# Optimization experiments

Hardware: AMD Instinct MI355X
Metric: run time of the kernel (lower is better)

## Reference

```python
import jax, jax.numpy as jnp
import numpy as np
from jax import lax

D, H, DK, L, FF, V, B, S = 384, 12, 32, 6, 1536, 30522, 16, 512

def _logit(p):
    return float(np.log(p / (1.0 - p)))

def setup_inputs():
    key = jax.random.key(0)
    ks = jax.random.split(key, 16)
    def g(i, shape, scale=0.02):
        return jax.random.normal(ks[i], shape, jnp.float32) * scale
    return {
        "input_ids": jax.random.randint(ks[0], (B, S), 0, V),
        "attention_mask": jnp.ones((B, S), jnp.int32),
        "emb_tok": g(1, (V, D)),
        "emb_pos": g(2, (S, D)),
        "emb_type": g(3, (2, D)),
        "emb_ln_g": jnp.ones((D,), jnp.float32),
        "emb_ln_b": jnp.zeros((D,), jnp.float32),
        "Wq": g(4, (L, D, D)), "bq": jnp.zeros((L, D), jnp.float32),
        "Wk": g(5, (L, D, D)), "bk": jnp.zeros((L, D), jnp.float32),
        "Wv": g(6, (L, D, D)), "bv": jnp.zeros((L, D), jnp.float32),
        "Wbeta": g(7, (L, D, H)), "bbeta": jnp.zeros((L, H), jnp.float32),
        "decay_fast": jnp.full((L, H), _logit(0.3), jnp.float32),
        "decay_slow": jnp.full((L, H), _logit(0.85), jnp.float32),
        "mix_logit": jnp.zeros((L, H), jnp.float32),
        "Wg": g(8, (L, D, D)),
        "Wo": g(9, (L, D, D)), "bo": jnp.zeros((L, D), jnp.float32),
        "attn_ln_g": jnp.ones((L, D), jnp.float32), "attn_ln_b": jnp.zeros((L, D), jnp.float32),
        "Wffn1": g(10, (L, D, FF)), "bffn1": jnp.zeros((L, FF), jnp.float32),
        "Wffn2": g(11, (L, FF, D)), "bffn2": jnp.zeros((L, D), jnp.float32),
        "ffn_ln_g": jnp.ones((L, D), jnp.float32), "ffn_ln_b": jnp.zeros((L, D), jnp.float32),
    }

def _ln(x, g, b, eps=1e-12):
    m = x.mean(-1, keepdims=True)
    v = ((x - m) ** 2).mean(-1, keepdims=True)
    return (x - m) * lax.rsqrt(v + eps) * g + b

def _delta_attn(x, mask_f, Wq, bq, Wk, bk, Wv, bv, Wbeta, bbeta, df_logit, ds_logit, mix_logit, Wg, Wo, bo):
    # Hierarchical delta-rule linear attention: O(n) recurrence, two decay timescales.
    Bz, Sq, _ = x.shape
    q = jax.nn.silu((x @ Wq + bq).reshape(Bz, Sq, H, DK))
    k = jax.nn.silu((x @ Wk + bk).reshape(Bz, Sq, H, DK))
    k = k / (jnp.linalg.norm(k, axis=-1, keepdims=True) + 1e-6)
    v = (x @ Wv + bv).reshape(Bz, Sq, H, DK)
    beta = jax.nn.sigmoid(x @ Wbeta + bbeta) * mask_f[..., None]  # [B,S,H]
    df = jax.nn.sigmoid(df_logit)[None, :, None, None]  # fast decay, per head
    ds = jax.nn.sigmoid(ds_logit)[None, :, None, None]  # slow decay, per head
    qT = q.transpose(1, 0, 2, 3)  # time-major [S,B,H,DK]
    kT = k.transpose(1, 0, 2, 3)
    vT = v.transpose(1, 0, 2, 3)
    betaT = beta.transpose(1, 0, 2)

    def step(carry, xs):
        Sf, Ss = carry  # [B,H,DK,DK] fast/slow memory states
        kt, vt, qt, bt = xs
        err_f = (vt - jnp.einsum('bhk,bhkv->bhv', kt, Sf)) * bt[..., None]
        Sf = df * Sf + jnp.einsum('bhk,bhv->bhkv', kt, err_f)
        err_s = (vt - jnp.einsum('bhk,bhkv->bhv', kt, Ss)) * bt[..., None]
        Ss = ds * Ss + jnp.einsum('bhk,bhv->bhkv', kt, err_s)
        of = jnp.einsum('bhk,bhkv->bhv', qt, Sf)
        os = jnp.einsum('bhk,bhkv->bhv', qt, Ss)
        return (Sf, Ss), (of, os)

    S0 = jnp.zeros((Bz, H, DK, DK), x.dtype)
    _, (ofT, osT) = lax.scan(step, (S0, S0), (kT, vT, qT, betaT))
    mix = jax.nn.sigmoid(mix_logit)[None, None, :, None]
    o = mix * ofT.transpose(1, 0, 2, 3) + (1.0 - mix) * osT.transpose(1, 0, 2, 3)
    o = o.reshape(Bz, Sq, D)
    o = o * jax.nn.sigmoid(x @ Wg)  # enhanced-flux output gate
    return o @ Wo + bo

def reference(input_ids, attention_mask, emb_tok, emb_pos, emb_type, emb_ln_g, emb_ln_b, Wq, bq, Wk, bk, Wv, bv, Wbeta, bbeta, decay_fast, decay_slow, mix_logit, Wg, Wo, bo, attn_ln_g, attn_ln_b, Wffn1, bffn1, Wffn2, bffn2, ffn_ln_g, ffn_ln_b):
    mask_f = attention_mask.astype(jnp.float32)
    h = emb_tok[input_ids] + emb_pos[None, :input_ids.shape[1]] + emb_type[0][None, None]
    h = _ln(h, emb_ln_g, emb_ln_b)
    for i in range(L):
        attn = _delta_attn(h, mask_f, Wq[i], bq[i], Wk[i], bk[i], Wv[i], bv[i], Wbeta[i], bbeta[i], decay_fast[i], decay_slow[i], mix_logit[i], Wg[i], Wo[i], bo[i])
        h = _ln(h + attn, attn_ln_g[i], attn_ln_b[i])
        ffn = jax.nn.gelu(h @ Wffn1[i] + bffn1[i], approximate=False) @ Wffn2[i] + bffn2[i]
        h = _ln(h + ffn, ffn_ln_g[i], ffn_ln_b[i])
    m = mask_f[..., None]
    emb = (h * m).sum(1) / jnp.clip(m.sum(1), 1e-9)
    return emb / (jnp.linalg.norm(emb, axis=1, keepdims=True) + 1e-12)
```

## Files before the change

kernel.cpp:

```cpp
#include <hip/hip_runtime.h>
#include <hip/hip_bf16.h>

#define NTOK   8192
#define DMODEL 384
#define NHEAD  12
#define DHEAD  32
#define NLAYER 6
#define DFF    1536
#define SEQ    512
#define BATCH  16
#define WTAL   1916928L

typedef __attribute__((ext_vector_type(8))) short short8;
typedef __attribute__((ext_vector_type(4))) float f32x4;

__device__ __forceinline__ float sigmoidf_(float x){ return 1.f/(1.f+expf(-x)); }

__device__ __forceinline__ ushort f2b(float x){
  uint b = __builtin_bit_cast(uint, x);
  uint r = (b + 0x7FFFu + ((b>>16)&1u)) >> 16;
  return (ushort)r;
}
__device__ __forceinline__ uint pk2(float lo, float hi){
  return (uint)f2b(lo) | ((uint)f2b(hi)<<16);
}
__device__ __forceinline__ float4 b2f4(uint2 u){
  float4 f;
  f.x = __builtin_bit_cast(float, u.x<<16);
  f.y = __builtin_bit_cast(float, u.x & 0xffff0000u);
  f.z = __builtin_bit_cast(float, u.y<<16);
  f.w = __builtin_bit_cast(float, u.y & 0xffff0000u);
  return f;
}
__device__ __forceinline__ float red8(float x){
  int t = __builtin_amdgcn_update_dpp(0, __builtin_bit_cast(int,x), 0xB1, 0xF, 0xF, true);
  x += __builtin_bit_cast(float,t);
  t = __builtin_amdgcn_update_dpp(0, __builtin_bit_cast(int,x), 0x4E, 0xF, 0xF, true);
  x += __builtin_bit_cast(float,t);
  t = __builtin_amdgcn_update_dpp(0, __builtin_bit_cast(int,x), 0x141, 0xF, 0xF, true);
  x += __builtin_bit_cast(float,t);
  return x;
}
__device__ __forceinline__ void gload16(const ushort* g, ushort* l){
  __builtin_amdgcn_global_load_lds((const __attribute__((address_space(1))) void*)g,
                                   (__attribute__((address_space(3))) void*)l, 16, 0, 0);
}

__global__ __launch_bounds__(128) void embed_ln_kernel(
    const int* __restrict__ ids, const float* __restrict__ tok,
    const float* __restrict__ pos, const float* __restrict__ typ,
    const float* __restrict__ g, const float* __restrict__ bvec,
    float* __restrict__ out, ushort* __restrict__ outb)
{
  int n = blockIdx.x;
  int t = n & (SEQ-1);
  int id = ids[n];
  int tid = threadIdx.x;
  float v[3]; float s1=0.f, s2=0.f;
  #pragma unroll
  for (int j=0;j<3;j++){
    int d = tid + j*128;
    float x = tok[(long)id*DMODEL + d] + pos[t*DMODEL + d] + typ[d];
    v[j]=x; s1+=x; s2+=x*x;
  }
  #pragma unroll
  for (int m=1;m<64;m<<=1){ s1 += __shfl_xor(s1,m); s2 += __shfl_xor(s2,m); }
  __shared__ float r1[2], r2[2];
  if ((tid&63)==0){ r1[tid>>6]=s1; r2[tid>>6]=s2; }
  __syncthreads();
  s1 = r1[0]+r1[1]; s2 = r2[0]+r2[1];
  float mean = s1*(1.f/DMODEL);
  float var  = s2*(1.f/DMODEL) - mean*mean;
  float inv  = rsqrtf(var + 1e-12f);
  #pragma unroll
  for (int j=0;j<3;j++){
    int d = tid + j*128;
    float y = (v[j]-mean)*inv*g[d] + bvec[d];
    out[(long)n*DMODEL + d] = y;
    outb[(long)n*DMODEL + d] = f2b(y);
  }
}

__global__ __launch_bounds__(128) void add_ln_kernel(
    float* __restrict__ h, const float* __restrict__ res,
    const float* __restrict__ g, const float* __restrict__ bvec,
    ushort* __restrict__ hb)
{
  int n = blockIdx.x;
  int tid = threadIdx.x;
  float v[3]; float s1=0.f, s2=0.f;
  #pragma unroll
  for (int j=0;j<3;j++){
    int d = tid + j*128;
    float x = h[(long)n*DMODEL + d] + res[(long)n*DMODEL + d];
    v[j]=x; s1+=x; s2+=x*x;
  }
  #pragma unroll
  for (int m=1;m<64;m<<=1){ s1 += __shfl_xor(s1,m); s2 += __shfl_xor(s2,m); }
  __shared__ float r1[2], r2[2];
  if ((tid&63)==0){ r1[tid>>6]=s1; r2[tid>>6]=s2; }
  __syncthreads();
  s1 = r1[0]+r1[1]; s2 = r2[0]+r2[1];
  float mean = s1*(1.f/DMODEL);
  float var  = s2*(1.f/DMODEL) - mean*mean;
  float inv  = rsqrtf(var + 1e-12f);
  #pragma unroll
  for (int j=0;j<3;j++){
    int d = tid + j*128;
    float y = (v[j]-mean)*inv*g[d] + bvec[d];
    h[(long)n*DMODEL + d] = y;
    hb[(long)n*DMODEL + d] = f2b(y);
  }
}

__global__ __launch_bounds__(256) void tcvt6(
    const float* __restrict__ Wq, const float* __restrict__ Wk,
    const float* __restrict__ Wv, const float* __restrict__ Wg,
    const float* __restrict__ Wo, const float* __restrict__ W1,
    const float* __restrict__ W2, ushort* __restrict__ WTA)
{
  __shared__ float tile[32][33];
  int l = blockIdx.x / 1872;
  int bid = blockIdx.x % 1872;
  const float* Wq_l = Wq + (long)l*DMODEL*DMODEL;
  const float* Wk_l = Wk + (long)l*DMODEL*DMODEL;
  const float* Wv_l = Wv + (long)l*DMODEL*DMODEL;
  const float* Wg_l = Wg + (long)l*DMODEL*DMODEL;
  const float* Wo_l = Wo + (long)l*DMODEL*DMODEL;
  const float* W1_l = W1 + (long)l*DMODEL*DFF;
  const float* W2_l = W2 + (long)l*DFF*DMODEL;
  ushort* WTAl = WTA + (long)l*WTAL;

  const float* src; long dstbase; int rowlen, Nd, tk, tn, row0;
  if (bid < 720){
    int seg = bid/144, t = bid%144;
    tk = t%12; tn = t/12;
    src = (seg==0)?Wq_l:(seg==1)?Wk_l:(seg==2)?Wv_l:(seg==3)?Wg_l:Wo_l;
    Nd = 384; rowlen = 384;
    if (seg<4){ dstbase=0; row0=seg*384; }
    else      { dstbase=589824; row0=0; }
  } else if (bid < 1296){
    int t = bid-720; tk=t%12; tn=t/12;
    src=W1_l; Nd=DFF; dstbase=737280; row0=0; rowlen=384;
  } else {
    int t = bid-1296; tk=t%48; tn=t/48;
    src=W2_l; Nd=384; dstbase=1327104; row0=0; rowlen=DFF;
  }
  int k0=tk*32, n0=tn*32;
  int tt=threadIdx.x;
  int r=tt>>3, c4=(tt&7)<<2;
  const float* sp = src + (long)(k0+r)*Nd + n0 + c4;
  float4 f = *(const float4*)sp;
  tile[r][c4+0]=f.x; tile[r][c4+1]=f.y; tile[r][c4+2]=f.z; tile[r][c4+3]=f.w;
  __syncthreads();
  ushort4 o;
  o.x=f2b(tile[c4+0][r]); o.y=f2b(tile[c4+1][r]);
  o.z=f2b(tile[c4+2][r]); o.w=f2b(tile[c4+3][r]);
  *(ushort4*)(WTAl + dstbase + (long)(row0+n0+r)*rowlen + k0 + c4) = o;
}

__device__ __forceinline__ int2 xcd_swz(){
  int lin = blockIdx.y*64 + blockIdx.x;
  int nb = gridDim.x*gridDim.y;
  int s = (lin & 7)*(nb>>3) + (lin>>3);
  return make_int2(s & 63, s >> 6);
}

template<int ACT, int OUTBF>
__global__ __launch_bounds__(256) void gemm_bf(
    const ushort* __restrict__ Xb, const ushort* __restrict__ WT,
    const float* __restrict__ bias, void* __restrict__ Cv, int Kd, int Nd)
{
  __shared__ ushort A_lds[128*32];
  __shared__ ushort B_lds[128*32];
  int tid = threadIdx.x;
  int2 bxy = xcd_swz();
  int bm = bxy.x*128, bn = bxy.y*128;
  int w = tid>>6, lane = tid&63;
  int wm = w>>1, wn = w&1;
  f32x4 acc[4][4];
  #pragma unroll
  for (int i=0;i<4;i++)
    #pragma unroll
    for (int j=0;j<4;j++) acc[i][j]=(f32x4)(0.f);

  int cl = lane&15, koff = (lane>>4)*8;
  int srow = w*32 + (lane>>2);
  int scol = (lane&3)*8;
  const ushort* gA0 = Xb + (long)(bm+srow)*Kd + scol;
  const ushort* gA1 = gA0 + 16*(long)Kd;
  const ushort* gB0 = WT + (long)(bn+srow)*Kd + scol;
  const ushort* gB1 = gB0 + 16*(long)Kd;
  ushort* lA = A_lds + w*1024;
  ushort* lB = B_lds + w*1024;

  for (int k0=0; k0<Kd; k0+=32){
    gload16(gA0+k0, lA);
    gload16(gA1+k0, lA+512);
    gload16(gB0+k0, lB);
    gload16(gB1+k0, lB+512);
    __syncthreads();
    short8 bf[4];
    #pragma unroll
    for (int ni=0;ni<4;ni++)
      bf[ni] = *(const short8*)&B_lds[(wn*64+ni*16+cl)*32 + koff];
    #pragma unroll
    for (int mi=0;mi<4;mi++){
      short8 af = *(const short8*)&A_lds[(wm*64+mi*16+cl)*32 + koff];
      #pragma unroll
      for (int ni=0;ni<4;ni++)
        acc[mi][ni] = __builtin_amdgcn_mfma_f32_16x16x32_bf16(af, bf[ni], acc[mi][ni], 0,0,0);
    }
    __syncthreads();
  }

  int rb = (lane>>4)*4;
  #pragma unroll
  for (int ni=0; ni<4; ni++){
    int col = bn + wn*64 + ni*16 + cl;
    float bsv = bias ? bias[col] : 0.f;
    #pragma unroll
    for (int mi=0; mi<4; mi++){
      #pragma unroll
      for (int j=0;j<4;j++){
        int row = bm + wm*64 + mi*16 + rb + j;
        float c = acc[mi][ni][j] + bsv;
        if (ACT==1)      c = c*sigmoidf_(c);
        else if (ACT==2) c = 0.5f*c*(1.f+erff(c*0.70710678118f));
        else if (ACT==3) c = sigmoidf_(c);
        if (OUTBF) ((ushort*)Cv)[(long)row*Nd + col] = f2b(c);
        else       ((float*)Cv)[(long)row*Nd + col] = c;
      }
    }
  }
}

template<int ACT, int OUTBF>
__global__ __launch_bounds__(256) void gemm_bf2(
    const ushort* __restrict__ Xb, const ushort* __restrict__ WT,
    const float* __restrict__ bias, void* __restrict__ Cv, int Kd, int Nd)
{
  __shared__ ushort A_lds[128*32];
  __shared__ ushort B_lds[64*32];
  int tid = threadIdx.x;
  int2 bxy = xcd_swz();
  int bm = bxy.x*128, bn = bxy.y*64;
  int w = tid>>6, lane = tid&63;
  int wm = w>>1, wn = w&1;
  f32x4 acc[4][2];
  #pragma unroll
  for (int i=0;i<4;i++){ acc[i][0]=(f32x4)(0.f); acc[i][1]=(f32x4)(0.f); }

  int cl = lane&15, koff = (lane>>4)*8;
  int srowA = w*32 + (lane>>2);
  int scol = (lane&3)*8;
  const ushort* gA0 = Xb + (long)(bm+srowA)*Kd + scol;
  const ushort* gA1 = gA0 + 16*(long)Kd;
  int srowB = w*16 + (lane>>2);
  const ushort* gB = WT + (long)(bn+srowB)*Kd + scol;
  ushort* lA = A_lds + w*1024;
  ushort* lB = B_lds + w*512;

  for (int k0=0; k0<Kd; k0+=32){
    gload16(gA0+k0, lA);
    gload16(gA1+k0, lA+512);
    gload16(gB+k0, lB);
    __syncthreads();
    short8 b0 = *(const short8*)&B_lds[(wn*32+cl)*32 + koff];
    short8 b1 = *(const short8*)&B_lds[(wn*32+16+cl)*32 + koff];
    #pragma unroll
    for (int mi=0;mi<4;mi++){
      short8 af = *(const short8*)&A_lds[(wm*64+mi*16+cl)*32 + koff];
      acc[mi][0] = __builtin_amdgcn_mfma_f32_16x16x32_bf16(af, b0, acc[mi][0], 0,0,0);
      acc[mi][1] = __builtin_amdgcn_mfma_f32_16x16x32_bf16(af, b1, acc[mi][1], 0,0,0);
    }
    __syncthreads();
  }

  int rb = (lane>>4)*4;
  #pragma unroll
  for (int ni=0; ni<2; ni++){
    int col = bn + wn*32 + ni*16 + cl;
    float bsv = bias ? bias[col] : 0.f;
    #pragma unroll
    for (int mi=0; mi<4; mi++){
      #pragma unroll
      for (int j=0;j<4;j++){
        int row = bm + wm*64 + mi*16 + rb + j;
        float c = acc[mi][ni][j] + bsv;
        if (ACT==1)      c = c*sigmoidf_(c);
        else if (ACT==2) c = 0.5f*c*(1.f+erff(c*0.70710678118f));
        else if (ACT==3) c = sigmoidf_(c);
        if (OUTBF) ((ushort*)Cv)[(long)row*Nd + col] = f2b(c);
        else       ((float*)Cv)[(long)row*Nd + col] = c;
      }
    }
  }
}

__global__ __launch_bounds__(256) void gemm_qkvg(
    const ushort* __restrict__ Xb, const ushort* __restrict__ WT,
    const float* __restrict__ bq, const float* __restrict__ bk,
    const float* __restrict__ bv, ushort* __restrict__ C)
{
  __shared__ ushort A_lds[128*32];
  __shared__ ushort B_lds[128*32];
  int tid = threadIdx.x;
  int2 bxy = xcd_swz();
  int bm = bxy.x*128, bn = bxy.y*128;
  int w = tid>>6, lane = tid&63;
  int wm = w>>1, wn = w&1;
  f32x4 acc[4][4];
  #pragma unroll
  for (int i=0;i<4;i++)
    #pragma unroll
    for (int j=0;j<4;j++) acc[i][j]=(f32x4)(0.f);

  int cl = lane&15, koff = (lane>>4)*8;
  int srow = w*32 + (lane>>2);
  int scol = (lane&3)*8;
  const ushort* gA0 = Xb + (long)(bm+srow)*DMODEL + scol;
  const ushort* gA1 = gA0 + 16*DMODEL;
  const ushort* gB0 = WT + (long)(bn+srow)*DMODEL + scol;
  const ushort* gB1 = gB0 + 16*DMODEL;
  ushort* lA = A_lds + w*1024;
  ushort* lB = B_lds + w*1024;

  for (int k0=0; k0<DMODEL; k0+=32){
    gload16(gA0+k0, lA);
    gload16(gA1+k0, lA+512);
    gload16(gB0+k0, lB);
    gload16(gB1+k0, lB+512);
    __syncthreads();
    short8 bf[4];
    #pragma unroll
    for (int ni=0;ni<4;ni++)
      bf[ni] = *(const short8*)&B_lds[(wn*64+ni*16+cl)*32 + koff];
    #pragma unroll
    for (int mi=0;mi<4;mi++){
      short8 af = *(const short8*)&A_lds[(wm*64+mi*16+cl)*32 + koff];
      #pragma unroll
      for (int ni=0;ni<4;ni++)
        acc[mi][ni] = __builtin_amdgcn_mfma_f32_16x16x32_bf16(af, bf[ni], acc[mi][ni], 0,0,0);
    }
    __syncthreads();
  }

  int seg = bxy.y/3;
  const float* bp = (seg==0)?bq:(seg==1)?bk:(seg==2)?bv:nullptr;
  int boff = seg*384;
  int rb = (lane>>4)*4;
  #pragma unroll
  for (int ni=0; ni<4; ni++){
    int col = bn + wn*64 + ni*16 + cl;
    float bsv = bp ? bp[col-boff] : 0.f;
    #pragma unroll
    for (int mi=0; mi<4; mi++){
      #pragma unroll
      for (int j=0;j<4;j++){
        int row = bm + wm*64 + mi*16 + rb + j;
        float c = acc[mi][ni][j] + bsv;
        if (seg<2)       c = c*sigmoidf_(c);
        else if (seg==3) c = sigmoidf_(c);
        C[(long)row*DFF + col] = f2b(c);
      }
    }
  }
}

__global__ __launch_bounds__(384) void beta_kernel(
    const float* __restrict__ X, const float* __restrict__ Wb, const float* __restrict__ bb,
    const int* __restrict__ mask, float* __restrict__ Bb)
{
  __shared__ float xs[DMODEL];
  int n = blockIdx.x; int tid = threadIdx.x;
  xs[tid] = X[(long)n*DMODEL + tid];
  __syncthreads();
  int hh = tid >> 5, i = tid & 31;
  float s = 0.f;
  for (int d=i; d<DMODEL; d+=32) s += xs[d]*Wb[d*NHEAD+hh];
  #pragma unroll
  for (int m=1;m<32;m<<=1) s += __shfl_xor(s,m);
  if (i==0) Bb[n*NHEAD+hh] = (float)mask[n] * sigmoidf_(s + bb[hh]);
}

__global__ __launch_bounds__(512,2) void scan12_kernel(
    const ushort* __restrict__ QKVGb, const float* __restrict__ Bb,
    const float* __restrict__ dfl, const float* __restrict__ dsl,
    const float* __restrict__ mixl, ushort* __restrict__ OA)
{
  __shared__ float Qc[66][36], Kc[66][36], Vt[32][68], Bc[68], Ofs[2][64][36];
  int bh = blockIdx.x;
  int b = bh / NHEAD, hh = bh - b*NHEAD;
  int tid = threadIdx.x;
  int w = tid>>6, lane = tid&63;
  int st = w>>2, vq = w&3;
  int kq = lane&7, v = vq*8 + (lane>>3);
  float dec = sigmoidf_(st ? dsl[hh] : dfl[hh]);
  float mix = sigmoidf_(mixl[hh]);
  long rowbase = (long)b*SEQ;
  const ushort* rp = QKVGb + rowbase*DFF + hh*32;
  const float* bp = Bb + rowbase*NHEAD + hh;

  int r0 = tid>>3, c40 = (tid&7)<<2;
  float S[4] = {0.f,0.f,0.f,0.f};

  float4 sq, sk, sv; float sb = 0.f;
  {
    long g = (long)r0*DFF;
    sq = b2f4(*(const uint2*)(rp + g + c40));
    sk = b2f4(*(const uint2*)(rp + g + 384 + c40));
    sv = b2f4(*(const uint2*)(rp + g + 768 + c40));
    if (tid < 64) sb = bp[(long)tid*NHEAD];
    float ss = red8(sk.x*sk.x + sk.y*sk.y + sk.z*sk.z + sk.w*sk.w);
    float inv = 1.f/(sqrtf(ss)+1e-6f);
    sk.x*=inv; sk.y*=inv; sk.z*=inv; sk.w*=inv;
    *(float4*)&Qc[r0][c40] = sq;
    *(float4*)&Kc[r0][c40] = sk;
    Vt[c40+0][r0]=sv.x; Vt[c40+1][r0]=sv.y; Vt[c40+2][r0]=sv.z; Vt[c40+3][r0]=sv.w;
    if (tid < 64) Bc[tid] = sb;
  }
  __syncthreads();

  for (int c=0; c<8; ++c){
    if (c < 7){
      long g = (long)((c+1)*64 + r0)*DFF;
      sq = b2f4(*(const uint2*)(rp + g + c40));
      sk = b2f4(*(const uint2*)(rp + g + 384 + c40));
      sv = b2f4(*(const uint2*)(rp + g + 768 + c40));
      if (tid < 64) sb = bp[(long)((c+1)*64 + tid)*NHEAD];
    }
    float4 g4 = b2f4(*(const uint2*)(rp + (long)(c*64 + r0)*DFF + 1152 + c40));
    __builtin_amdgcn_sched_barrier(0);

    float4 kA = *(const float4*)&Kc[0][kq*4];
    float4 qA = *(const float4*)&Qc[0][kq*4];
    float4 kB = *(const float4*)&Kc[1][kq*4];
    float4 qB = *(const float4*)&Qc[1][kq*4];
    float vrA[4], brA[4], vrB[4], brB[4];
    *(float4*)vrA = *(const float4*)&Vt[v][0];
    *(float4*)brA = *(const float4*)&Bc[0];

    for (int t8=0; t8<8; ++t8){
      *(float4*)vrB = *(const float4*)&Vt[v][(2*t8+1)*4];
      *(float4*)brB = *(const float4*)&Bc[(2*t8+1)*4];
      #pragma unroll
      for (int i=0;i<4;i++){
        int t = t8*8 + i;
        float4 kN = *(const float4*)&Kc[t+2][kq*4];
        float4 qN = *(const float4*)&Qc[t+2][kq*4];
        float pa = kA.x*S[0] + kA.y*S[1];
        float pb = kA.z*S[2] + kA.w*S[3];
        float p = red8(pa+pb);
        float err = (vrA[i] - p)*brA[i];
        S[0] = dec*S[0] + kA.x*err;
        S[1] = dec*S[1] + kA.y*err;
        S[2] = dec*S[2] + kA.z*err;
        S[3] = dec*S[3] + kA.w*err;
        float oa = qA.x*S[0] + qA.y*S[1];
        float ob = qA.z*S[2] + qA.w*S[3];
        float o = red8(oa+ob);
        if (kq==0) Ofs[st][t][v] = o;
        kA=kB; qA=qB; kB=kN; qB=qN;
      }
      *(float4*)vrA = *(const float4*)&Vt[v][(2*t8+2)*4];
      *(float4*)brA = *(const float4*)&Bc[(2*t8+2)*4];
      #pragma unroll
      for (int i=0;i<4;i++){
        int t = t8*8 + 4 + i;
        float4 kN = *(const float4*)&Kc[t+2][kq*4];
        float4 qN = *(const float4*)&Qc[t+2][kq*4];
        float pa = kA.x*S[0] + kA.y*S[1];
        float pb = kA.z*S[2] + kA.w*S[3];
        float p = red8(pa+pb);
        float err = (vrB[i] - p)*brB[i];
        S[0] = dec*S[0] + kA.x*err;
        S[1] = dec*S[1] + kA.y*err;
        S[2] = dec*S[2] + kA.z*err;
        S[3] = dec*S[3] + kA.w*err;
        float oa = qA.x*S[0] + qA.y*S[1];
        float ob = qA.z*S[2] + qA.w*S[3];
        float o = red8(oa+ob);
        if (kq==0) Ofs[st][t][v] = o;
        kA=kB; qA=qB; kB=kN; qB=qN;
      }
    }
    __syncthreads();

    {
      float4 of = *(const float4*)&Ofs[0][r0][c40];
      float4 os = *(const float4*)&Ofs[1][r0][c40];
      float a0 = (mix*of.x + (1.f-mix)*os.x)*g4.x;
      float a1 = (mix*of.y + (1.f-mix)*os.y)*g4.y;
      float a2 = (mix*of.z + (1.f-mix)*os.z)*g4.z;
      float a3 = (mix*of.w + (1.f-mix)*os.w)*g4.w;
      uint2 o2; o2.x = pk2(a0,a1); o2.y = pk2(a2,a3);
      *(uint2*)(OA + (rowbase + c*64 + r0)*DMODEL + hh*32 + c40) = o2;
    }
    if (c < 7){
      *(float4*)&Qc[r0][c40] = sq;
      *(float4*)&Kc[r0][c40] = sk;
      Vt[c40+0][r0]=sv.x; Vt[c40+1][r0]=sv.y; Vt[c40+2][r0]=sv.z; Vt[c40+3][r0]=sv.w;
      if (tid < 64) Bc[tid] = sb;
    }
    __syncthreads();
  }
}

__global__ __launch_bounds__(384) void pool_norm_kernel(
    const float* __restrict__ h, const int* __restrict__ mask, float* __restrict__ out)
{
  int b = blockIdx.x; int d = threadIdx.x;
  float s=0.f, ms=0.f;
  for (int t=0;t<SEQ;t++){
    float m = (float)mask[b*SEQ+t];
    s += h[((long)b*SEQ+t)*DMODEL + d]*m;
    ms += m;
  }
  float emb = s / fmaxf(ms, 1e-9f);
  float ss = emb*emb;
  #pragma unroll
  for (int m2=1;m2<64;m2<<=1) ss += __shfl_xor(ss,m2);
  __shared__ float r[6];
  if ((d&63)==0) r[d>>6]=ss;
  __syncthreads();
  ss = r[0]+r[1]+r[2]+r[3]+r[4]+r[5];
  out[b*DMODEL+d] = emb / (sqrtf(ss)+1e-12f);
}

extern "C" void kernel_launch(void* const* d_in, const int* in_sizes, int n_in,
                              void* d_out, int out_size, void* d_ws, size_t ws_size,
                              hipStream_t stream)
{
  const int*   ids   = (const int*)d_in[0];
  const int*   amask = (const int*)d_in[1];
  const float* etok  = (const float*)d_in[2];
  const float* epos  = (const float*)d_in[3];
  const float* etyp  = (const float*)d_in[4];
  const float* elng  = (const float*)d_in[5];
  const float* elnb  = (const float*)d_in[6];
  const float* Wq = (const float*)d_in[7];  const float* bq = (const float*)d_in[8];
  const float* Wk = (const float*)d_in[9];  const float* bk = (const float*)d_in[10];
  const float* Wv = (const float*)d_in[11]; const float* bv = (const float*)d_in[12];
  const float* Wb = (const float*)d_in[13]; const float* bb = (const float*)d_in[14];
  const float* dfl = (const float*)d_in[15];
  const float* dsl = (const float*)d_in[16];
  const float* mixl= (const float*)d_in[17];
  const float* Wg = (const float*)d_in[18];
  const float* Wo = (const float*)d_in[19]; const float* bo = (const float*)d_in[20];
  const float* alng = (const float*)d_in[21]; const float* alnb = (const float*)d_in[22];
  const float* W1 = (const float*)d_in[23]; const float* b1 = (const float*)d_in[24];
  const float* W2 = (const float*)d_in[25]; const float* b2 = (const float*)d_in[26];
  const float* flng = (const float*)d_in[27]; const float* flnb = (const float*)d_in[28];

  float* ws = (float*)d_ws;
  const long TD = (long)NTOK*DMODEL;
  float* h      = ws;
  ushort* hbf   = (ushort*)(h + TD);
  ushort* QKVGb = (ushort*)(h + TD + TD/2);
  ushort* OA    = (ushort*)(h + TD + TD/2 + 2*TD);
  float* Rb     = h + TD + TD/2 + 2*TD + TD/2;
  float* Bb     = Rb + TD;
  ushort* WTA   = (ushort*)(Bb + (long)NTOK*NHEAD);
  ushort* F1B   = QKVGb;

  embed_ln_kernel<<<NTOK,128,0,stream>>>(ids, etok, epos, etyp, elng, elnb, h, hbf);
  tcvt6<<<6*1872,256,0,stream>>>(Wq, Wk, Wv, Wg, Wo, W1, W2, WTA);

  for (int l=0;l<NLAYER;l++){
    ushort* WTAl = WTA + (long)l*WTAL;
    gemm_qkvg<<<dim3(64,12),256,0,stream>>>(hbf, WTAl, bq+l*DMODEL, bk+l*DMODEL, bv+l*DMODEL, QKVGb);
    beta_kernel<<<NTOK,384,0,stream>>>(h, Wb + (long)l*DMODEL*NHEAD, bb + l*NHEAD, amask, Bb);
    scan12_kernel<<<BATCH*NHEAD,512,0,stream>>>(QKVGb, Bb, dfl + l*NHEAD, dsl + l*NHEAD, mixl + l*NHEAD, OA);
    gemm_bf2<0,0><<<dim3(64,6),256,0,stream>>>(OA, WTAl+589824, bo + l*DMODEL, Rb, DMODEL, DMODEL);
    add_ln_kernel<<<NTOK,128,0,stream>>>(h, Rb, alng + (long)l*DMODEL, alnb + (long)l*DMODEL, hbf);
    gemm_bf<2,1><<<dim3(64,12),256,0,stream>>>(hbf, WTAl+737280, b1 + (long)l*DFF, F1B, DMODEL, DFF);
    gemm_bf2<0,0><<<dim3(64,6),256,0,stream>>>(F1B, WTAl+1327104, b2 + (long)l*DMODEL, Rb, DFF, DMODEL);
    add_ln_kernel<<<NTOK,128,0,stream>>>(h, Rb, flng + (long)l*DMODEL, flnb + (long)l*DMODEL, hbf);
  }

  pool_norm_kernel<<<BATCH,384,0,stream>>>(h, amask, (float*)d_out);
}
```

Measured before the change: 1.365 ms.

## Fuse beta projection into LayerNorm kernels and widen scan to 1024 threads

Removes the standalone beta kernel by computing the next layer's beta gate inside the embedding LayerNorm and the FFN add-LayerNorm, reusing the normalized row already in registers. The delta-rule scan kernel is doubled to 1024 threads so each lane holds 2 state elements instead of 4, with 16-lane DPP reductions, and the Q/V and K/beta chunk loads are split across the two halves. This is meant to cut a launch and a re-read of h per layer and to shorten the serial per-step dependency chain in the scan. In exchange, LayerNorm kernels take extra shared memory and a reduction step, and the scan uses more threads and a longer reduction per step.

```diff
diff --git a/kernel.cpp b/kernel.cpp
--- a/kernel.cpp
+++ b/kernel.cpp
@@ -41,17 +41,62 @@
   x += __builtin_bit_cast(float,t);
   return x;
 }
+__device__ __forceinline__ float red16(float x){
+  int t = __builtin_amdgcn_update_dpp(0, __builtin_bit_cast(int,x), 0xB1, 0xF, 0xF, true);
+  x += __builtin_bit_cast(float,t);
+  t = __builtin_amdgcn_update_dpp(0, __builtin_bit_cast(int,x), 0x4E, 0xF, 0xF, true);
+  x += __builtin_bit_cast(float,t);
+  t = __builtin_amdgcn_update_dpp(0, __builtin_bit_cast(int,x), 0x141, 0xF, 0xF, true);
+  x += __builtin_bit_cast(float,t);
+  t = __builtin_amdgcn_update_dpp(0, __builtin_bit_cast(int,x), 0x140, 0xF, 0xF, true);
+  x += __builtin_bit_cast(float,t);
+  return x;
+}
 __device__ __forceinline__ void gload16(const ushort* g, ushort* l){
   __builtin_amdgcn_global_load_lds((const __attribute__((address_space(1))) void*)g,
                                    (__attribute__((address_space(3))) void*)l, 16, 0, 0);
+}
+
+__device__ __forceinline__ void beta_from_row(
+    int n, int tid, const float y0, const float y1, const float y2,
+    const float* __restrict__ Wb, const float* __restrict__ bbv,
+    const int* __restrict__ amask, float* __restrict__ Bb,
+    float (*bred)[13])
+{
+  float part[12];
+  #pragma unroll
+  for (int hh=0;hh<12;hh++) part[hh]=0.f;
+  #pragma unroll
+  for (int j=0;j<3;j++){
+    int d = tid + j*128;
+    float yv = (j==0)?y0:(j==1)?y1:y2;
+    const float* wrow = Wb + (long)d*12;
+    #pragma unroll
+    for (int hh=0;hh<12;hh++) part[hh] += yv * wrow[hh];
+  }
+  #pragma unroll
+  for (int hh=0;hh<12;hh++) bred[tid][hh] = part[hh];
+  __syncthreads();
+  if (tid < 96){
+    int hh = tid>>3, i = tid&7;
+    float s = 0.f;
+    #pragma unroll
+    for (int k=0;k<16;k++) s += bred[i + 8*k][hh];
+    s += __shfl_xor(s,1); s += __shfl_xor(s,2); s += __shfl_xor(s,4);
+    if (i==0) Bb[(long)n*NHEAD+hh] = (float)amask[n] * sigmoidf_(s + bbv[hh]);
+  }
 }
 
 __global__ __launch_bounds__(128) void embed_ln_kernel(
     const int* __restrict__ ids, const float* __restrict__ tok,
     const float* __restrict__ pos, const float* __restrict__ typ,
     const float* __restrict__ g, const float* __restrict__ bvec,
-    float* __restrict__ out, ushort* __restrict__ outb)
-{
+    float* __restrict__ out, ushort* __restrict__ outb,
+    const float* __restrict__ Wb0, const float* __restrict__ bb0,
+    const int* __restrict__ amask, float* __restrict__ Bb)
+{
+  __shared__ float r1[2], r2[2];
+  __shared__ float bred[128][13];
   int n = blockIdx.x;
   int t = n & (SEQ-1);
   int id = ids[n];
@@ -65,27 +110,33 @@
   }
   #pragma unroll
   for (int m=1;m<64;m<<=1){ s1 += __shfl_xor(s1,m); s2 += __shfl_xor(s2,m); }
-  __shared__ float r1[2], r2[2];
   if ((tid&63)==0){ r1[tid>>6]=s1; r2[tid>>6]=s2; }
   __syncthreads();
   s1 = r1[0]+r1[1]; s2 = r2[0]+r2[1];
   float mean = s1*(1.f/DMODEL);
   float var  = s2*(1.f/DMODEL) - mean*mean;
   float inv  = rsqrtf(var + 1e-12f);
+  float y[3];
   #pragma unroll
   for (int j=0;j<3;j++){
     int d = tid + j*128;
-    float y = (v[j]-mean)*inv*g[d] + bvec[d];
-    out[(long)n*DMODEL + d] = y;
-    outb[(long)n*DMODEL + d] = f2b(y);
-  }
+    y[j] = (v[j]-mean)*inv*g[d] + bvec[d];
+    out[(long)n*DMODEL + d] = y[j];
+    outb[(long)n*DMODEL + d] = f2b(y[j]);
+  }
+  __syncthreads();
+  beta_from_row(n, tid, y[0], y[1], y[2], Wb0, bb0, amask, Bb, bred);
 }
 
 __global__ __launch_bounds__(128) void add_ln_kernel(
     float* __restrict__ h, const float* __restrict__ res,
     const float* __restrict__ g, const float* __restrict__ bvec,
-    ushort* __restrict__ hb)
-{
+    ushort* __restrict__ hb,
+    const float* __restrict__ Wbn, const float* __restrict__ bbn,
+    const int* __restrict__ amask, float* __restrict__ Bb)
+{
+  __shared__ float r1[2], r2[2];
+  __shared__ float bred[128][13];
   int n = blockIdx.x;
   int tid = threadIdx.x;
   float v[3]; float s1=0.f, s2=0.f;
@@ -97,19 +148,23 @@
   }
   #pragma unroll
   for (int m=1;m<64;m<<=1){ s1 += __shfl_xor(s1,m); s2 += __shfl_xor(s2,m); }
-  __shared__ float r1[2], r2[2];
   if ((tid&63)==0){ r1[tid>>6]=s1; r2[tid>>6]=s2; }
   __syncthreads();
   s1 = r1[0]+r1[1]; s2 = r2[0]+r2[1];
   float mean = s1*(1.f/DMODEL);
   float var  = s2*(1.f/DMODEL) - mean*mean;
   float inv  = rsqrtf(var + 1e-12f);
+  float y[3];
   #pragma unroll
   for (int j=0;j<3;j++){
     int d = tid + j*128;
-    float y = (v[j]-mean)*inv*g[d] + bvec[d];
-    h[(long)n*DMODEL + d] = y;
-    hb[(long)n*DMODEL + d] = f2b(y);
+    y[j] = (v[j]-mean)*inv*g[d] + bvec[d];
+    h[(long)n*DMODEL + d] = y[j];
+    hb[(long)n*DMODEL + d] = f2b(y[j]);
+  }
+  if (Wbn){
+    __syncthreads();
+    beta_from_row(n, tid, y[0], y[1], y[2], Wbn, bbn, amask, Bb, bred);
   }
 }
 
@@ -368,23 +423,7 @@
   }
 }
 
-__global__ __launch_bounds__(384) void beta_kernel(
-    const float* __restrict__ X, const float* __restrict__ Wb, const float* __restrict__ bb,
-    const int* __restrict__ mask, float* __restrict__ Bb)
-{
-  __shared__ float xs[DMODEL];
-  int n = blockIdx.x; int tid = threadIdx.x;
-  xs[tid] = X[(long)n*DMODEL + tid];
-  __syncthreads();
-  int hh = tid >> 5, i = tid & 31;
-  float s = 0.f;
-  for (int d=i; d<DMODEL; d+=32) s += xs[d]*Wb[d*NHEAD+hh];
-  #pragma unroll
-  for (int m=1;m<32;m<<=1) s += __shfl_xor(s,m);
-  if (i==0) Bb[n*NHEAD+hh] = (float)mask[n] * sigmoidf_(s + bb[hh]);
-}
-
-__global__ __launch_bounds__(512,2) void scan12_kernel(
+__global__ __launch_bounds__(1024,4) void scan14_kernel(
     const ushort* __restrict__ QKVGb, const float* __restrict__ Bb,
     const float* __restrict__ dfl, const float* __restrict__ dsl,
     const float* __restrict__ mixl, ushort* __restrict__ OA)
@@ -394,49 +433,58 @@
   int b = bh / NHEAD, hh = bh - b*NHEAD;
   int tid = threadIdx.x;
   int w = tid>>6, lane = tid&63;
-  int st = w>>2, vq = w&3;
-  int kq = lane&7, v = vq*8 + (lane>>3);
+  int st = w>>3, vg = w&7;
+  int kq = lane&15, v = vg*4 + (lane>>4);
   float dec = sigmoidf_(st ? dsl[hh] : dfl[hh]);
-  float mix = sigmoidf_(mixl[hh]);
+  float mixv = sigmoidf_(mixl[hh]);
   long rowbase = (long)b*SEQ;
   const ushort* rp = QKVGb + rowbase*DFF + hh*32;
   const float* bp = Bb + rowbase*NHEAD + hh;
 
-  int r0 = tid>>3, c40 = (tid&7)<<2;
-  float S[4] = {0.f,0.f,0.f,0.f};
+  bool sideA = tid < 512;
+  int ts = sideA ? tid : (tid-512);
+  int r0 = ts>>3, c40 = (ts&7)<<2;
+  float S0=0.f, S1=0.f;
 
   float4 sq, sk, sv; float sb = 0.f;
   {
     long g = (long)r0*DFF;
-    sq = b2f4(*(const uint2*)(rp + g + c40));
-    sk = b2f4(*(const uint2*)(rp + g + 384 + c40));
-    sv = b2f4(*(const uint2*)(rp + g + 768 + c40));
-    if (tid < 64) sb = bp[(long)tid*NHEAD];
-    float ss = red8(sk.x*sk.x + sk.y*sk.y + sk.z*sk.z + sk.w*sk.w);
-    float inv = 1.f/(sqrtf(ss)+1e-6f);
-    sk.x*=inv; sk.y*=inv; sk.z*=inv; sk.w*=inv;
-    *(float4*)&Qc[r0][c40] = sq;
-    *(float4*)&Kc[r0][c40] = sk;
-    Vt[c40+0][r0]=sv.x; Vt[c40+1][r0]=sv.y; Vt[c40+2][r0]=sv.z; Vt[c40+3][r0]=sv.w;
-    if (tid < 64) Bc[tid] = sb;
+    if (sideA){
+      sq = b2f4(*(const uint2*)(rp + g + c40));
+      sv = b2f4(*(const uint2*)(rp + g + 768 + c40));
+      *(float4*)&Qc[r0][c40] = sq;
+      Vt[c40+0][r0]=sv.x; Vt[c40+1][r0]=sv.y; Vt[c40+2][r0]=sv.z; Vt[c40+3][r0]=sv.w;
+    } else {
+      sk = b2f4(*(const uint2*)(rp + g + 384 + c40));
+      if (ts < 64) sb = bp[(long)ts*NHEAD];
+      float ss = red8(sk.x*sk.x + sk.y*sk.y + sk.z*sk.z + sk.w*sk.w);
+      float inv = 1.f/(sqrtf(ss)+1e-6f);
+      sk.x*=inv; sk.y*=inv; sk.z*=inv; sk.w*=inv;
+      *(float4*)&Kc[r0][c40] = sk;
+      if (ts < 64) Bc[ts] = sb;
+    }
   }
   __syncthreads();
 
   for (int c=0; c<8; ++c){
+    float4 g4;
     if (c < 7){
       long g = (long)((c+1)*64 + r0)*DFF;
-      sq = b2f4(*(const uint2*)(rp + g + c40));
-      sk = b2f4(*(const uint2*)(rp + g + 384 + c40));
-      sv = b2f4(*(const uint2*)(rp + g + 768 + c40));
-      if (tid < 64) sb = bp[(long)((c+1)*64 + tid)*NHEAD];
-    }
-    float4 g4 = b2f4(*(const uint2*)(rp + (long)(c*64 + r0)*DFF + 1152 + c40));
+      if (sideA){
+        sq = b2f4(*(const uint2*)(rp + g + c40));
+        sv = b2f4(*(const uint2*)(rp + g + 768 + c40));
+      } else {
+        sk = b2f4(*(const uint2*)(rp + g + 384 + c40));
+        if (ts < 64) sb = bp[(long)((c+1)*64 + ts)*NHEAD];
+      }
+    }
+    if (!sideA) g4 = b2f4(*(const uint2*)(rp + (long)(c*64 + r0)*DFF + 1152 + c40));
     __builtin_amdgcn_sched_barrier(0);
 
-    float4 kA = *(const float4*)&Kc[0][kq*4];
-    float4 qA = *(const float4*)&Qc[0][kq*4];
-    float4 kB = *(const float4*)&Kc[1][kq*4];
-    float4 qB = *(const float4*)&Qc[1][kq*4];
+    float2 kA = *(const float2*)&Kc[0][kq*2];
+    float2 qA = *(const float2*)&Qc[0][kq*2];
+    float2 kB = *(const float2*)&Kc[1][kq*2];
+    float2 qB = *(const float2*)&Qc[1][kq*2];
     float vrA[4], brA[4], vrB[4], brB[4];
     *(float4*)vrA = *(const float4*)&Vt[v][0];
     *(float4*)brA = *(const float4*)&Bc[0];
@@ -447,19 +495,13 @@
       #pragma unroll
       for (int i=0;i<4;i++){
         int t = t8*8 + i;
-        float4 kN = *(const float4*)&Kc[t+2][kq*4];
-        float4 qN = *(const float4*)&Qc[t+2][kq*4];
-        float pa = kA.x*S[0] + kA.y*S[1];
-        float pb = kA.z*S[2] + kA.w*S[3];
-        float p = red8(pa+pb);
+        float2 kN = *(const float2*)&Kc[t+2][kq*2];
+        float2 qN = *(const float2*)&Qc[t+2][kq*2];
+        float p = red16(kA.x*S0 + kA.y*S1);
         float err = (vrA[i] - p)*brA[i];
-        S[0] = dec*S[0] + kA.x*err;
-        S[1] = dec*S[1] + kA.y*err;
-        S[2] = dec*S[2] + kA.z*err;
-        S[3] = dec*S[3] + kA.w*err;
-        float oa = qA.x*S[0] + qA.y*S[1];
-        float ob = qA.z*S[2] + qA.w*S[3];
-        float o = red8(oa+ob);
+        S0 = dec*S0 + kA.x*err;
+        S1 = dec*S1 + kA.y*err;
+        float o = red16(qA.x*S0 + qA.y*S1);
         if (kq==0) Ofs[st][t][v] = o;
         kA=kB; qA=qB; kB=kN; qB=qN;
       }
@@ -468,40 +510,37 @@
       #pragma unroll
       for (int i=0;i<4;i++){
         int t = t8*8 + 4 + i;
-        float4 kN = *(const float4*)&Kc[t+2][kq*4];
-        float4 qN = *(const float4*)&Qc[t+2][kq*4];
-        float pa = kA.x*S[0] + kA.y*S[1];
-        float pb = kA.z*S[2] + kA.w*S[3];
-        float p = red8(pa+pb);
+        float2 kN = *(const float2*)&Kc[t+2][kq*2];
+        float2 qN = *(const float2*)&Qc[t+2][kq*2];
+        float p = red16(kA.x*S0 + kA.y*S1);
         float err = (vrB[i] - p)*brB[i];
-        S[0] = dec*S[0] + kA.x*err;
-        S[1] = dec*S[1] + kA.y*err;
-        S[2] = dec*S[2] + kA.z*err;
-        S[3] = dec*S[3] + kA.w*err;
-        float oa = qA.x*S[0] + qA.y*S[1];
-        float ob = qA.z*S[2] + qA.w*S[3];
-        float o = red8(oa+ob);
+        S0 = dec*S0 + kA.x*err;
+        S1 = dec*S1 + kA.y*err;
+        float o = red16(qA.x*S0 + qA.y*S1);
         if (kq==0) Ofs[st][t][v] = o;
         kA=kB; qA=qB; kB=kN; qB=qN;
       }
     }
     __syncthreads();
 
-    {
+    if (!sideA){
       float4 of = *(const float4*)&Ofs[0][r0][c40];
       float4 os = *(const float4*)&Ofs[1][r0][c40];
-      float a0 = (mix*of.x + (1.f-mix)*os.x)*g4.x;
-      float a1 = (mix*of.y + (1.f-mix)*os.y)*g4.y;
-      float a2 = (mix*of.z + (1.f-mix)*os.z)*g4.z;
-      float a3 = (mix*of.w + (1.f-mix)*os.w)*g4.w;
+      float a0 = (mixv*of.x + (1.f-mixv)*os.x)*g4.x;
+      float a1 = (mixv*of.y + (1.f-mixv)*os.y)*g4.y;
+      float a2 = (mixv*of.z + (1.f-mixv)*os.z)*g4.z;
+      float a3 = (mixv*of.w + (1.f-mixv)*os.w)*g4.w;
       uint2 o2; o2.x = pk2(a0,a1); o2.y = pk2(a2,a3);
       *(uint2*)(OA + (rowbase + c*64 + r0)*DMODEL + hh*32 + c40) = o2;
     }
     if (c < 7){
-      *(float4*)&Qc[r0][c40] = sq;
-      *(float4*)&Kc[r0][c40] = sk;
-      Vt[c40+0][r0]=sv.x; Vt[c40+1][r0]=sv.y; Vt[c40+2][r0]=sv.z; Vt[c40+3][r0]=sv.w;
-      if (tid < 64) Bc[tid] = sb;
+      if (sideA){
+        *(float4*)&Qc[r0][c40] = sq;
+        Vt[c40+0][r0]=sv.x; Vt[c40+1][r0]=sv.y; Vt[c40+2][r0]=sv.z; Vt[c40+3][r0]=sv.w;
+      } else {
+        *(float4*)&Kc[r0][c40] = sk;
+        if (ts < 64) Bc[ts] = sb;
+      }
     }
     __syncthreads();
   }
@@ -564,19 +603,23 @@
   ushort* WTA   = (ushort*)(Bb + (long)NTOK*NHEAD);
   ushort* F1B   = QKVGb;
 
-  embed_ln_kernel<<<NTOK,128,0,stream>>>(ids, etok, epos, etyp, elng, elnb, h, hbf);
+  embed_ln_kernel<<<NTOK,128,0,stream>>>(ids, etok, epos, etyp, elng, elnb, h, hbf,
+                                         Wb, bb, amask, Bb);
   tcvt6<<<6*1872,256,0,stream>>>(Wq, Wk, Wv, Wg, Wo, W1, W2, WTA);
 
   for (int l=0;l<NLAYER;l++){
     ushort* WTAl = WTA + (long)l*WTAL;
     gemm_qkvg<<<dim3(64,12),256,0,stream>>>(hbf, WTAl, bq+l*DMODEL, bk+l*DMODEL, bv+l*DMODEL, QKVGb);
-    beta_kernel<<<NTOK,384,0,stream>>>(h, Wb + (long)l*DMODEL*NHEAD, bb + l*NHEAD, amask, Bb);
-    scan12_kernel<<<BATCH*NHEAD,512,0,stream>>>(QKVGb, Bb, dfl + l*NHEAD, dsl + l*NHEAD, mixl + l*NHEAD, OA);
+    scan14_kernel<<<BATCH*NHEAD,1024,0,stream>>>(QKVGb, Bb, dfl + l*NHEAD, dsl + l*NHEAD, mixl + l*NHEAD, OA);
     gemm_bf2<0,0><<<dim3(64,6),256,0,stream>>>(OA, WTAl+589824, bo + l*DMODEL, Rb, DMODEL, DMODEL);
-    add_ln_kernel<<<NTOK,128,0,stream>>>(h, Rb, alng + (long)l*DMODEL, alnb + (long)l*DMODEL, hbf);
+    add_ln_kernel<<<NTOK,128,0,stream>>>(h, Rb, alng + (long)l*DMODEL, alnb + (long)l*DMODEL, hbf,
+                                         nullptr, nullptr, amask, Bb);
     gemm_bf<2,1><<<dim3(64,12),256,0,stream>>>(hbf, WTAl+737280, b1 + (long)l*DFF, F1B, DMODEL, DFF);
     gemm_bf2<0,0><<<dim3(64,6),256,0,stream>>>(F1B, WTAl+1327104, b2 + (long)l*DMODEL, Rb, DFF, DMODEL);
-    add_ln_kernel<<<NTOK,128,0,stream>>>(h, Rb, flng + (long)l*DMODEL, flnb + (long)l*DMODEL, hbf);
+    const float* Wbn = (l+1<NLAYER) ? (Wb + (long)(l+1)*DMODEL*NHEAD) : nullptr;
+    const float* bbn = (l+1<NLAYER) ? (bb + (long)(l+1)*NHEAD) : nullptr;
+    add_ln_kernel<<<NTOK,128,0,stream>>>(h, Rb, flng + (long)l*DMODEL, flnb + (long)l*DMODEL, hbf,
+                                         Wbn, bbn, amask, Bb);
   }
 
   pool_norm_kernel<<<BATCH,384,0,stream>>>(h, amask, (float*)d_out);
```

Result: faster. 1.259 ms (-7.8%).
